# Optimization experiments

Hardware: AMD Instinct MI355X
Metric: run time of the kernel (lower is better)

## Reference

```python
import jax, jax.numpy as jnp
from jax import lax
import numpy as np

B, S, H, L = 128, 256, 768, 24


def setup_inputs() -> dict:
    key = jax.random.key(0)
    k_tf, k_len, k_w, k_tr, k_st, k_en = jax.random.split(key, 6)
    token_features = jax.random.normal(k_tf, (B, S, H), dtype=jnp.float32)
    # contiguous valid lengths in [3, S] (>=3 so that stripping CLS/SEP leaves >=1 token)
    lengths = jax.random.randint(k_len, (B,), 3, S + 1)
    pos = jnp.arange(S)
    input_mask = (pos[None, :] < lengths[:, None]).astype(jnp.int32)
    true_label_mask = (pos[None, :] < (lengths - 2)[:, None]).astype(jnp.int32)
    W = jax.random.normal(k_w, (H, L), dtype=jnp.float32) * 0.02
    b = jnp.zeros((L,), dtype=jnp.float32)
    transitions = jax.random.normal(k_tr, (L, L), dtype=jnp.float32) * 0.1
    start_trans = jax.random.normal(k_st, (L,), dtype=jnp.float32) * 0.1
    end_trans = jax.random.normal(k_en, (L,), dtype=jnp.float32) * 0.1
    return {
        "token_features": token_features,
        "input_mask": input_mask,
        "true_label_mask": true_label_mask,
        "W": W,
        "b": b,
        "transitions": transitions,
        "start_trans": start_trans,
        "end_trans": end_trans,
    }


def _compact(x, mask):
    """Vectorized version of the torch per-token copy loop: for each row,
    gather valid tokens (mask==1) preserving order, drop the first and last
    valid token (CLS/SEP), left-pack into a zero tensor."""
    # stable argsort puts valid positions first, in order
    order = jnp.argsort(1 - mask.astype(jnp.int32), axis=1)  # [B,S]
    gathered = jnp.take_along_axis(x, order[:, :, None], axis=1)  # [B,S,H]
    # drop first valid token (shift left by 1), pad a zero row at the end
    shifted = jnp.concatenate([gathered[:, 1:], jnp.zeros_like(gathered[:, :1])], axis=1)
    n_valid = mask.sum(axis=1)  # [B]
    keep = jnp.arange(x.shape[1])[None, :] < (n_valid[:, None] - 2)  # also drops last (SEP)
    return jnp.where(keep[:, :, None], shifted, 0.0)


def _viterbi(emissions, mask, transitions, start_trans, end_trans):
    """Masked Viterbi decode. emissions [B,S,L], mask [B,S] bool."""
    Bn, Sn, Ln = emissions.shape
    lbl = jnp.arange(Ln)
    score0 = start_trans[None, :] + emissions[:, 0]  # [B,L]

    def step(score, xs):
        em_t, m_t = xs  # [B,L], [B]
        cand = score[:, :, None] + transitions[None]  # [B,prev,curr]
        best = cand.max(axis=1) + em_t
        bp = cand.argmax(axis=1)  # [B,L] best prev tag per curr tag
        new_score = jnp.where(m_t[:, None], best, score)
        bp = jnp.where(m_t[:, None], bp, lbl[None, :])  # identity backpointer on pad
        return new_score, bp

    ems = jnp.swapaxes(emissions[:, 1:], 0, 1)  # [S-1,B,L]
    ms = jnp.swapaxes(mask[:, 1:], 0, 1)  # [S-1,B]
    final, bps = lax.scan(step, score0, (ems, ms))
    final = final + end_trans[None, :]
    best_score = final.max(axis=1)  # [B]
    last_tag = final.argmax(axis=1)  # [B]

    def back(tag, bp):  # tag: tag at time t; bp: bp_t -> tag at t-1
        prev = jnp.take_along_axis(bp, tag[:, None], axis=1)[:, 0]
        return prev, tag

    tag0, tags_rest = lax.scan(back, last_tag, bps, reverse=True)  # tags_rest [S-1,B]
    path = jnp.concatenate([tag0[:, None], jnp.swapaxes(tags_rest, 0, 1)], axis=1)  # [B,S]
    return best_score, path


def reference(token_features, input_mask, true_label_mask, W, b, transitions, start_trans, end_trans):
    mask = input_mask.astype(bool)
    wv = _compact(token_features, mask)  # dropout is identity at inference
    emissions = jax.nn.sigmoid(wv @ W + b)  # [B,S,L]
    _, path = _viterbi(emissions, true_label_mask != 0, transitions, start_trans, end_trans)
    return path
```

## Files before the change

kernel.cpp:

```cpp
#include <hip/hip_runtime.h>
#include <hip/hip_bf16.h>
#include <math.h>

#define NB 128
#define NS 256
#define NH 768
#define NL 24

__global__ __launch_bounds__(256) void ner_emis(
    const float* __restrict__ tf, const int* __restrict__ tlm,
    const float* __restrict__ W, const float* __restrict__ bias,
    float* __restrict__ E)
{
    const int b    = blockIdx.x >> 2;
    const int tile = (blockIdx.x & 3) << 6;
    const int tid  = threadIdx.x;
    if (tlm[b*NS + tile] == 0) return;

    __shared__ float As[64*129];
    __shared__ float Ps[4*64*NL];

    const int lane = tid & 63;
    const int w    = __builtin_amdgcn_readfirstlane(tid >> 6);

    float acc[NL];
    #pragma unroll
    for (int l = 0; l < NL; ++l) acc[l] = 0.f;

    const float* tfb = tf + (size_t)(b*NS)*NH;

    for (int kc0 = 0; kc0 < NH; kc0 += 128) {
        #pragma unroll
        for (int i = 0; i < 8; ++i) {
            int idx  = tid + (i << 8);
            int row  = idx >> 5;
            int c4   = idx & 31;
            int trow = tile + row + 1;
            if (trow > 255) trow = 255;
            float4 v = *(const float4*)(tfb + (size_t)trow*NH + kc0 + (c4 << 2));
            float* dst = As + row*129 + (c4 << 2);
            dst[0] = v.x; dst[1] = v.y; dst[2] = v.z; dst[3] = v.w;
        }
        __syncthreads();

        const int kbase = kc0 + (w << 5);
        #pragma unroll
        for (int k = 0; k < 32; ++k) {
            float a = As[lane*129 + (w << 5) + k];
            const float* wr = W + (size_t)(kbase + k)*NL;
            #pragma unroll
            for (int l = 0; l < NL; ++l) acc[l] = fmaf(a, wr[l], acc[l]);
        }
        __syncthreads();
    }

    {
        float* p = Ps + (w*64 + lane)*NL;
        #pragma unroll
        for (int l = 0; l < NL; ++l) p[l] = acc[l];
    }
    __syncthreads();

    const int* tm = tlm + b*NS + tile;
    float* Eb = E + (size_t)(b*NS + tile)*NL;
    #pragma unroll
    for (int j = 0; j < 6; ++j) {
        int idx = tid + (j << 8);
        int tok = idx / NL, l = idx % NL;
        if (tm[tok]) {
            float s = Ps[(0*64 + tok)*NL + l] + Ps[(1*64 + tok)*NL + l]
                    + Ps[(2*64 + tok)*NL + l] + Ps[(3*64 + tok)*NL + l];
            float x = s + bias[l];
            Eb[tok*NL + l] = 1.0f/(1.0f + expf(-x));
        }
    }
}

__global__ __launch_bounds__(256) void ner_viterbi(
    const float* __restrict__ E, const int* __restrict__ tlm,
    const float* __restrict__ trans, const float* __restrict__ st,
    const float* __restrict__ en, int* __restrict__ out)
{
    const int tid = threadIdx.x;
    const int b   = blockIdx.x;
    const int bS  = b*NS;

    __shared__ float Esh[NS*NL];
    __shared__ float scl[NS*NL];
    __shared__ float Tt[NL*NL];
    __shared__ float fin[NL];
    __shared__ unsigned char tr_s[NL][NS];
    __shared__ int chosen[12];
    __shared__ int nsh, ltag;

    {
        const float4* src = (const float4*)(E + (size_t)bS*NL);
        float4* dst = (float4*)Esh;
        #pragma unroll
        for (int j = 0; j < 6; ++j) dst[tid + (j << 8)] = src[tid + (j << 8)];
    }
    for (int i = tid; i < NL*NL; i += 256) {
        int c = i / NL, p = i % NL;
        Tt[i] = trans[p*NL + c];
    }
    if (tid < 64) {
        int a = tlm[bS+tid] + tlm[bS+tid+64] + tlm[bS+tid+128] + tlm[bS+tid+192];
        #pragma unroll
        for (int off = 32; off > 0; off >>= 1) a += __shfl_down(a, off, 64);
        if (tid == 0) nsh = a;
    }
    __syncthreads();
    const int n = nsh;

    if (tid < 64) {
        const int c = tid % 24;
        float Tc[24];
        #pragma unroll
        for (int p = 0; p < 24; ++p) Tc[p] = trans[p*NL + c];

        auto rl = [](float v, int p) {
            return __int_as_float(__builtin_amdgcn_readlane(__float_as_int(v), p));
        };

        float sv = st[c] + Esh[c];
        scl[c] = sv;
        float scr[24];
        #pragma unroll
        for (int p = 0; p < 24; ++p) scr[p] = rl(sv, p);

        float emn = Esh[NL + c];
        for (int t = 1; t < n; ++t) {
            float em = emn;
            int tn = (t+1 < n-1) ? t+1 : n-1;
            emn = Esh[tn*NL + c];
            float cand[24];
            #pragma unroll
            for (int p = 0; p < 24; ++p) cand[p] = scr[p] + Tc[p];
            float m0 = fmaxf(fmaxf(cand[0],  cand[1]),  cand[2]);
            float m1 = fmaxf(fmaxf(cand[3],  cand[4]),  cand[5]);
            float m2 = fmaxf(fmaxf(cand[6],  cand[7]),  cand[8]);
            float m3 = fmaxf(fmaxf(cand[9],  cand[10]), cand[11]);
            float m4 = fmaxf(fmaxf(cand[12], cand[13]), cand[14]);
            float m5 = fmaxf(fmaxf(cand[15], cand[16]), cand[17]);
            float m6 = fmaxf(fmaxf(cand[18], cand[19]), cand[20]);
            float m7 = fmaxf(fmaxf(cand[21], cand[22]), cand[23]);
            float q0 = fmaxf(fmaxf(m0, m1), m2);
            float q1 = fmaxf(fmaxf(m3, m4), m5);
            float q2 = fmaxf(m6, m7);
            float best = fmaxf(fmaxf(q0, q1), q2);
            sv = best + em;
            scl[t*NL + c] = sv;
            #pragma unroll
            for (int p = 0; p < 24; ++p) scr[p] = rl(sv, p);
        }
        fin[c] = sv + en[c];
    }
    __syncthreads();

    if (tid == 0) {
        float bv = fin[0]; int bt = 0;
        #pragma unroll
        for (int cc = 1; cc < 24; ++cc) { if (fin[cc] > bv) { bv = fin[cc]; bt = cc; } }
        ltag = bt;
    }
    __syncthreads();

    const int K = (n > 1) ? (n - 1 + 9) / 10 : 1;
    if (n > 1 && tid < 240) {
        const int w = tid / 24 + 1, h = tid % 24;
        int tlo = (w-1)*K; if (tlo > n-1) tlo = n-1;
        int thi = w*K;     if (thi > n-1) thi = n-1;
        int cur = h;
        for (int t = thi; t > tlo; --t) {
            const float4* sp = (const float4*)(scl + (t-1)*NL);
            const float4* up = (const float4*)(Tt  + cur*NL);
            float cand[24];
            #pragma unroll
            for (int i = 0; i < 6; ++i) {
                float4 s = sp[i], u = up[i];
                cand[4*i+0] = s.x + u.x;
                cand[4*i+1] = s.y + u.y;
                cand[4*i+2] = s.z + u.z;
                cand[4*i+3] = s.w + u.w;
            }
            float best = cand[0]; int arg = 0;
            #pragma unroll
            for (int p = 1; p < 24; ++p) { if (cand[p] > best) { best = cand[p]; arg = p; } }
            tr_s[h][t-1] = (unsigned char)arg;
            cur = arg;
        }
    }
    __syncthreads();

    if (tid == 0) {
        int cur = ltag;
        for (int w = 10; w >= 1; --w) {
            chosen[w] = cur;
            int tlo = (w-1)*K; if (tlo > n-1) tlo = n-1;
            int thi = w*K;     if (thi > n-1) thi = n-1;
            if (thi > tlo) cur = tr_s[cur][tlo];
        }
    }
    __syncthreads();

    {
        const int t = tid;
        int tag;
        if (t >= n-1) tag = ltag;
        else { int w = t / K + 1; tag = tr_s[chosen[w]][t]; }
        out[bS + t] = tag;
    }
}

extern "C" void kernel_launch(void* const* d_in, const int* in_sizes, int n_in,
                              void* d_out, int out_size, void* d_ws, size_t ws_size,
                              hipStream_t stream) {
    const float* tf    = (const float*)d_in[0];
    const int*   tlm   = (const int*)  d_in[2];
    const float* W     = (const float*)d_in[3];
    const float* bias  = (const float*)d_in[4];
    const float* trans = (const float*)d_in[5];
    const float* st    = (const float*)d_in[6];
    const float* en    = (const float*)d_in[7];
    float* E = (float*)d_ws;

    ner_emis<<<dim3(NB*4), dim3(256), 0, stream>>>(tf, tlm, W, bias, E);
    ner_viterbi<<<dim3(NB), dim3(256), 0, stream>>>(E, tlm, trans, st, en, (int*)d_out);
}
```

Measured before the change: 239.3 us.

## Shrink emission K-chunk to cut LDS use; batch-prefetch emissions in Viterbi loop

The emission GEMM now stages 64-wide K chunks instead of 128, so each wave handles 16 k values per chunk. The partial sums are reduced through a smaller padded shared buffer with a two-step pairwise reduction, which lowers LDS footprint and should allow more blocks per CU. The Viterbi forward loop is restructured to load 8 emissions at a time ahead of the serial dependency chain. The cost is more chunk iterations and barriers, plus the extra reduction syncs.

```diff
diff --git a/kernel.cpp b/kernel.cpp
--- a/kernel.cpp
+++ b/kernel.cpp
@@ -17,11 +17,12 @@
     const int tid  = threadIdx.x;
     if (tlm[b*NS + tile] == 0) return;
 
-    __shared__ float As[64*129];
-    __shared__ float Ps[4*64*NL];
+    __shared__ float As[64*65];
+    __shared__ float P2[2*64*25];
 
     const int lane = tid & 63;
     const int w    = __builtin_amdgcn_readfirstlane(tid >> 6);
+    const int koff = w << 4;
 
     float acc[NL];
     #pragma unroll
@@ -29,33 +30,44 @@
 
     const float* tfb = tf + (size_t)(b*NS)*NH;
 
-    for (int kc0 = 0; kc0 < NH; kc0 += 128) {
-        #pragma unroll
-        for (int i = 0; i < 8; ++i) {
+    for (int kc0 = 0; kc0 < NH; kc0 += 64) {
+        #pragma unroll
+        for (int i = 0; i < 4; ++i) {
             int idx  = tid + (i << 8);
-            int row  = idx >> 5;
-            int c4   = idx & 31;
+            int row  = idx >> 4;
+            int c4   = idx & 15;
             int trow = tile + row + 1;
             if (trow > 255) trow = 255;
             float4 v = *(const float4*)(tfb + (size_t)trow*NH + kc0 + (c4 << 2));
-            float* dst = As + row*129 + (c4 << 2);
+            float* dst = As + row*65 + (c4 << 2);
             dst[0] = v.x; dst[1] = v.y; dst[2] = v.z; dst[3] = v.w;
         }
         __syncthreads();
 
-        const int kbase = kc0 + (w << 5);
-        #pragma unroll
-        for (int k = 0; k < 32; ++k) {
-            float a = As[lane*129 + (w << 5) + k];
-            const float* wr = W + (size_t)(kbase + k)*NL;
+        #pragma unroll
+        for (int k = 0; k < 16; ++k) {
+            float a = As[lane*65 + koff + k];
+            const float* wr = W + (size_t)(kc0 + koff + k)*NL;
             #pragma unroll
             for (int l = 0; l < NL; ++l) acc[l] = fmaf(a, wr[l], acc[l]);
         }
         __syncthreads();
     }
 
-    {
-        float* p = Ps + (w*64 + lane)*NL;
+    if (w & 1) {
+        float* p = P2 + ((w >> 1)*64 + lane)*25;
+        #pragma unroll
+        for (int l = 0; l < NL; ++l) p[l] = acc[l];
+    }
+    __syncthreads();
+    if (!(w & 1)) {
+        const float* p = P2 + ((w >> 1)*64 + lane)*25;
+        #pragma unroll
+        for (int l = 0; l < NL; ++l) acc[l] += p[l];
+    }
+    __syncthreads();
+    if (!(w & 1)) {
+        float* p = P2 + ((w >> 1)*64 + lane)*25;
         #pragma unroll
         for (int l = 0; l < NL; ++l) p[l] = acc[l];
     }
@@ -68,8 +80,7 @@
         int idx = tid + (j << 8);
         int tok = idx / NL, l = idx % NL;
         if (tm[tok]) {
-            float s = Ps[(0*64 + tok)*NL + l] + Ps[(1*64 + tok)*NL + l]
-                    + Ps[(2*64 + tok)*NL + l] + Ps[(3*64 + tok)*NL + l];
+            float s = P2[(0*64 + tok)*25 + l] + P2[(1*64 + tok)*25 + l];
             float x = s + bias[l];
             Eb[tok*NL + l] = 1.0f/(1.0f + expf(-x));
         }
@@ -128,11 +139,7 @@
         #pragma unroll
         for (int p = 0; p < 24; ++p) scr[p] = rl(sv, p);
 
-        float emn = Esh[NL + c];
-        for (int t = 1; t < n; ++t) {
-            float em = emn;
-            int tn = (t+1 < n-1) ? t+1 : n-1;
-            emn = Esh[tn*NL + c];
+        auto step = [&](int t, float em) {
             float cand[24];
             #pragma unroll
             for (int p = 0; p < 24; ++p) cand[p] = scr[p] + Tc[p];
@@ -152,7 +159,18 @@
             scl[t*NL + c] = sv;
             #pragma unroll
             for (int p = 0; p < 24; ++p) scr[p] = rl(sv, p);
-        }
+        };
+
+        int t = 1;
+        for (; t + 8 <= n; t += 8) {
+            float em[8];
+            const float* eb = Esh + t*NL + c;
+            #pragma unroll
+            for (int j = 0; j < 8; ++j) em[j] = eb[j*NL];
+            #pragma unroll
+            for (int j = 0; j < 8; ++j) step(t + j, em[j]);
+        }
+        for (; t < n; ++t) step(t, Esh[t*NL + c]);
         fin[c] = sv + en[c];
     }
     __syncthreads();
```

Result: faster. 226.4 us (-5.4%).
